# Kernel tuning notes

Hardware: AMD Instinct MI355X
Metric: run time of the kernel (lower is better)

## Reference

```python
import jax, jax.numpy as jnp
import numpy as np

HW = 1048576   # h*w pixels (1024x1024)
C = 64         # feature channels
K = 4096       # number of superpixel clusters (min_superpixels)
H1 = 256       # KAN hidden width
NCLS = 16      # output classes
G = 5          # grid_size
SO = 3         # spline_order


def _grid(in_features):
    # torch: (arange(-SO, G+SO+1) * h + grid_range[0]).expand(in_features, -1)
    h = 2.0 / G  # (grid_range[1]-grid_range[0])/grid_size
    g = jnp.arange(-SO, G + SO + 1, dtype=jnp.float32) * h - 1.0  # [G+2*SO+1]
    return jnp.broadcast_to(g, (in_features, G + 2 * SO + 1))


def _b_splines(x, grid):
    # x: [N, in] -> bases: [N, in, G+SO]
    xg = x[:, :, None]
    bases = ((xg >= grid[:, :-1]) & (xg < grid[:, 1:])).astype(x.dtype)
    for k in range(1, SO + 1):
        left = (xg - grid[:, :-(k + 1)]) / (grid[:, k:-1] - grid[:, :-(k + 1)])
        right = (grid[:, k + 1:] - xg) / (grid[:, k + 1:] - grid[:, 1:-k])
        bases = left * bases[:, :, :-1] + right * bases[:, :, 1:]
    return bases


def _kan_layer(x, base_w, spline_w, spline_scaler):
    # KANLinear.forward: silu(x) @ base_w.T + bsplines(x) . (spline_w * scaler)
    grid = _grid(x.shape[-1])
    base_out = jax.nn.silu(x) @ base_w.T                      # [N, out]
    bases = _b_splines(x, grid)                               # [N, in, G+SO]
    scaled_w = spline_w * spline_scaler[:, :, None]           # [out, in, G+SO]
    spline_out = jnp.einsum('nig,oig->no', bases, scaled_w)
    return base_out + spline_out


def setup_inputs() -> dict:
    key = jax.random.key(0)
    ks = jax.random.split(key, 8)
    x = jax.random.normal(ks[0], (HW, C), dtype=jnp.float32)
    cls = jax.random.randint(ks[1], (HW,), 0, K, dtype=jnp.int32)
    bw1 = jax.random.normal(ks[2], (H1, C), dtype=jnp.float32) * 0.1
    sw1 = jax.random.normal(ks[3], (H1, C, G + SO), dtype=jnp.float32) * 0.1
    sc1 = jax.random.normal(ks[4], (H1, C), dtype=jnp.float32) * 0.1
    bw2 = jax.random.normal(ks[5], (NCLS, H1), dtype=jnp.float32) * 0.1
    sw2 = jax.random.normal(ks[6], (NCLS, H1, G + SO), dtype=jnp.float32) * 0.1
    sc2 = jax.random.normal(ks[7], (NCLS, H1), dtype=jnp.float32) * 0.1
    return dict(x=x, cls=cls, bw1=bw1, sw1=sw1, sc1=sc1, bw2=bw2, sw2=sw2, sc2=sc2)


def reference(x, cls, bw1, sw1, sc1, bw2, sw2, sc2):
    # VDSM scatter-mean aggregation: per-cluster mean of pixel features
    sums = jax.ops.segment_sum(x, cls, num_segments=K)                       # [K, C]
    cnt = jax.ops.segment_sum(jnp.ones((HW,), x.dtype), cls, num_segments=K)  # [K]
    clus_feat = sums / jnp.maximum(cnt, 1.0)[:, None]
    # WIC_Cls: stack of KANLinear layers on cluster features
    h = _kan_layer(clus_feat, bw1, sw1, sc1)
    out = _kan_layer(h, bw2, sw2, sc2)
    return out
```

## Files before the change

kernel.cpp:

```cpp
#include <hip/hip_runtime.h>

#define HW_N 1048576
#define C_IN 64
#define K_CLS 4096
#define H1_N 256
#define NCLS_N 16
#define SCAT_BLOCKS 256
#define ROWS_PER_SCAT (HW_N / SCAT_BLOCKS)
#define CAP 512
#define CLPB 8

__device__ __forceinline__ float silu_f(float x) {
  return x / (1.0f + expf(-x));
}

__device__ __forceinline__ void bspline8(float x, float* b) {
  float t[11];
#pragma unroll
  for (int j = 0; j < 11; ++j) {
    float g0 = 0.4f * (float)(j - 3) - 1.0f;
    float g1 = 0.4f * (float)(j - 2) - 1.0f;
    t[j] = (x >= g0 && x < g1) ? 1.0f : 0.0f;
  }
#pragma unroll
  for (int k = 1; k <= 3; ++k) {
#pragma unroll 10
    for (int j = 0; j + k < 11; ++j) {
      float gj   = 0.4f * (float)(j - 3) - 1.0f;
      float gj1  = 0.4f * (float)(j - 2) - 1.0f;
      float gjk  = 0.4f * (float)(j + k - 3) - 1.0f;
      float gjk1 = 0.4f * (float)(j + k - 2) - 1.0f;
      float left  = (x - gj) / (gjk - gj);
      float right = (gjk1 - x) / (gjk1 - gj1);
      t[j] = left * t[j] + right * t[j + 1];
    }
  }
#pragma unroll
  for (int g = 0; g < 8; ++g) b[g] = t[g];
}

__global__ __launch_bounds__(256) void transpose_w(
    const float* __restrict__ bw1, const float* __restrict__ sw1,
    const float* __restrict__ sc1, const float* __restrict__ bw2,
    const float* __restrict__ sw2, const float* __restrict__ sc2,
    float* __restrict__ bwt1, float* __restrict__ swt1,
    float* __restrict__ bwt2, float* __restrict__ swt2,
    int* __restrict__ ccnt) {
  int bid = blockIdx.x, tid = threadIdx.x;
  if (bid < C_IN) {
    int i = bid, o = tid;
    float sc = sc1[o * C_IN + i];
    bwt1[i * H1_N + o] = bw1[o * C_IN + i];
    const float4* src = (const float4*)&sw1[(size_t)(o * C_IN + i) * 8];
    float4 a = src[0], b = src[1];
    a.x *= sc; a.y *= sc; a.z *= sc; a.w *= sc;
    b.x *= sc; b.y *= sc; b.z *= sc; b.w *= sc;
    float4* dst = (float4*)&swt1[(size_t)(i * H1_N + o) * 8];
    dst[0] = a; dst[1] = b;
  } else if (bid < C_IN + H1_N / 2) {
    int gi = (bid - C_IN) * 2 + (tid >> 7);
    int t = tid & 127;
    int o = t >> 3, e = t & 7;
    swt2[(gi * NCLS_N + o) * 8 + e] =
        sw2[(size_t)(o * H1_N + gi) * 8 + e] * sc2[o * H1_N + gi];
    if (t < NCLS_N) bwt2[gi * NCLS_N + t] = bw2[t * H1_N + gi];
  } else {
    ccnt[(bid - C_IN - H1_N / 2) * 256 + tid] = 0;
  }
}

__global__ __launch_bounds__(1024) void scatter_atomic(
    const int* __restrict__ cls, int* __restrict__ ccnt,
    int* __restrict__ spk) {
  __shared__ int lhist[K_CLS];
  int b = blockIdx.x, tid = threadIdx.x;
  for (int c = tid; c < K_CLS; c += 1024) lhist[c] = 0;
  __syncthreads();
  int r0 = b * ROWS_PER_SCAT;
  for (int r = r0 + tid; r < r0 + ROWS_PER_SCAT; r += 1024)
    atomicAdd(&lhist[cls[r]], 1);
  __syncthreads();
  for (int c = tid; c < K_CLS; c += 1024) {
    int n = lhist[c];
    lhist[c] = n ? atomicAdd(&ccnt[c], n) : 0;
  }
  __syncthreads();
  for (int r = r0 + tid; r < r0 + ROWS_PER_SCAT; r += 1024) {
    int c = cls[r];
    int pos = atomicAdd(&lhist[c], 1);
    spk[(size_t)c * CAP + pos] = r;
  }
}

__global__ __launch_bounds__(512, 4) void mega(
    const float* __restrict__ x, const int* __restrict__ spk,
    const int* __restrict__ ccnt, const float* __restrict__ bwt1,
    const float* __restrict__ swt1, const float* __restrict__ bwt2,
    const float* __restrict__ swt2, float* __restrict__ out) {
  __shared__ float s_bases[8][516];
  __shared__ float s_silu[8][65];
  __shared__ float mean_sacc[8][65];
  __shared__ float h_lds[8][257];
  __shared__ int sn[8];

  int bid = blockIdx.x, tid = threadIdx.x;
  int wv = tid >> 6, lane = tid & 63;
  int g = lane >> 4, q = lane & 15;

  if (tid < CLPB) sn[tid] = ccnt[bid * CLPB + tid];
  __syncthreads();

  {
    int n = sn[wv];
    const int* sid = spk + (size_t)(bid * CLPB + wv) * CAP;
    const float4* x4 = (const float4*)x;
    float ax = 0.0f, ay = 0.0f, az = 0.0f, aw = 0.0f;
    int i = g;
    for (; i + 28 < n; i += 32) {
      int p0 = sid[i],      p1 = sid[i + 4],  p2 = sid[i + 8],  p3 = sid[i + 12];
      int p4 = sid[i + 16], p5 = sid[i + 20], p6 = sid[i + 24], p7 = sid[i + 28];
      float4 v0 = x4[(size_t)p0 * 16 + q];
      float4 v1 = x4[(size_t)p1 * 16 + q];
      float4 v2 = x4[(size_t)p2 * 16 + q];
      float4 v3 = x4[(size_t)p3 * 16 + q];
      float4 v4 = x4[(size_t)p4 * 16 + q];
      float4 v5 = x4[(size_t)p5 * 16 + q];
      float4 v6 = x4[(size_t)p6 * 16 + q];
      float4 v7 = x4[(size_t)p7 * 16 + q];
      float tx0 = v0.x + v1.x, tx1 = v2.x + v3.x, tx2 = v4.x + v5.x, tx3 = v6.x + v7.x;
      float ty0 = v0.y + v1.y, ty1 = v2.y + v3.y, ty2 = v4.y + v5.y, ty3 = v6.y + v7.y;
      float tz0 = v0.z + v1.z, tz1 = v2.z + v3.z, tz2 = v4.z + v5.z, tz3 = v6.z + v7.z;
      float tw0 = v0.w + v1.w, tw1 = v2.w + v3.w, tw2 = v4.w + v5.w, tw3 = v6.w + v7.w;
      ax += (tx0 + tx1) + (tx2 + tx3);
      ay += (ty0 + ty1) + (ty2 + ty3);
      az += (tz0 + tz1) + (tz2 + tz3);
      aw += (tw0 + tw1) + (tw2 + tw3);
    }
    if (i < n) {
      int nm1 = n - 1;
      int i1 = i + 4, i2 = i + 8, i3 = i + 12, i4 = i + 16, i5 = i + 20,
          i6 = i + 24, i7 = i + 28;
      int p0 = sid[i];
      int p1 = sid[i1 < nm1 ? i1 : nm1];
      int p2 = sid[i2 < nm1 ? i2 : nm1];
      int p3 = sid[i3 < nm1 ? i3 : nm1];
      int p4 = sid[i4 < nm1 ? i4 : nm1];
      int p5 = sid[i5 < nm1 ? i5 : nm1];
      int p6 = sid[i6 < nm1 ? i6 : nm1];
      int p7 = sid[i7 < nm1 ? i7 : nm1];
      float4 v0 = x4[(size_t)p0 * 16 + q];
      float4 v1 = x4[(size_t)p1 * 16 + q];
      float4 v2 = x4[(size_t)p2 * 16 + q];
      float4 v3 = x4[(size_t)p3 * 16 + q];
      float4 v4 = x4[(size_t)p4 * 16 + q];
      float4 v5 = x4[(size_t)p5 * 16 + q];
      float4 v6 = x4[(size_t)p6 * 16 + q];
      float4 v7 = x4[(size_t)p7 * 16 + q];
      ax += v0.x; ay += v0.y; az += v0.z; aw += v0.w;
      if (i1 < n) { ax += v1.x; ay += v1.y; az += v1.z; aw += v1.w; }
      if (i2 < n) { ax += v2.x; ay += v2.y; az += v2.z; aw += v2.w; }
      if (i3 < n) { ax += v3.x; ay += v3.y; az += v3.z; aw += v3.w; }
      if (i4 < n) { ax += v4.x; ay += v4.y; az += v4.z; aw += v4.w; }
      if (i5 < n) { ax += v5.x; ay += v5.y; az += v5.z; aw += v5.w; }
      if (i6 < n) { ax += v6.x; ay += v6.y; az += v6.z; aw += v6.w; }
      if (i7 < n) { ax += v7.x; ay += v7.y; az += v7.z; aw += v7.w; }
    }
    ax += __shfl_xor(ax, 16); ax += __shfl_xor(ax, 32);
    ay += __shfl_xor(ay, 16); ay += __shfl_xor(ay, 32);
    az += __shfl_xor(az, 16); az += __shfl_xor(az, 32);
    aw += __shfl_xor(aw, 16); aw += __shfl_xor(aw, 32);
    if (g == 0) {
      float inv = 1.0f / fmaxf((float)n, 1.0f);
      mean_sacc[wv][q * 4 + 0] = ax * inv;
      mean_sacc[wv][q * 4 + 1] = ay * inv;
      mean_sacc[wv][q * 4 + 2] = az * inv;
      mean_sacc[wv][q * 4 + 3] = aw * inv;
    }
  }
  __syncthreads();

  {
    int r = tid >> 6, i = tid & 63;
    float xv = mean_sacc[r][i];
    s_silu[r][i] = silu_f(xv);
    float b[8];
    bspline8(xv, b);
    float4* dst = (float4*)&s_bases[r][i * 8];
    dst[0] = make_float4(b[0], b[1], b[2], b[3]);
    dst[1] = make_float4(b[4], b[5], b[6], b[7]);
  }
  __syncthreads();

  {
    int o = tid & 255, ih = tid >> 8;
    float acc[8];
#pragma unroll
    for (int r = 0; r < 8; ++r) acc[r] = 0.0f;
    int i0 = ih * 32;
    for (int i = i0; i < i0 + 32; ++i) {
      float wb = bwt1[i * H1_N + o];
      const float4* wp = (const float4*)&swt1[(size_t)(i * H1_N + o) * 8];
      float4 w0 = wp[0], w1 = wp[1];
#pragma unroll
      for (int r = 0; r < 8; ++r) {
        float sv = s_silu[r][i];
        const float4* bp = (const float4*)&s_bases[r][i * 8];
        float4 b0 = bp[0], b1 = bp[1];
        float a = acc[r];
        a = fmaf(sv, wb, a);
        a = fmaf(b0.x, w0.x, a); a = fmaf(b0.y, w0.y, a);
        a = fmaf(b0.z, w0.z, a); a = fmaf(b0.w, w0.w, a);
        a = fmaf(b1.x, w1.x, a); a = fmaf(b1.y, w1.y, a);
        a = fmaf(b1.z, w1.z, a); a = fmaf(b1.w, w1.w, a);
        acc[r] = a;
      }
    }
    if (ih == 0) {
#pragma unroll
      for (int r = 0; r < 8; ++r) h_lds[r][o] = acc[r];
    }
    __syncthreads();
    if (ih == 1) {
#pragma unroll
      for (int r = 0; r < 8; ++r) h_lds[r][o] += acc[r];
    }
  }
  __syncthreads();

  {
    int o2 = tid & 15, rr = (tid >> 4) & 7, jh = tid >> 7;
    float acc2 = 0.0f;
    for (int ic0 = 0; ic0 < H1_N; ic0 += 64) {
      {
        int r = tid >> 6, i = tid & 63;
        float xv = h_lds[r][ic0 + i];
        s_silu[r][i] = silu_f(xv);
        float b[8];
        bspline8(xv, b);
        float4* dst = (float4*)&s_bases[r][i * 8];
        dst[0] = make_float4(b[0], b[1], b[2], b[3]);
        dst[1] = make_float4(b[4], b[5], b[6], b[7]);
      }
      __syncthreads();
      int ib = jh * 16;
      for (int i = ib; i < ib + 16; ++i) {
        int gi = ic0 + i;
        float wb = bwt2[gi * NCLS_N + o2];
        const float4* wp = (const float4*)&swt2[(gi * NCLS_N + o2) * 8];
        float4 w0 = wp[0], w1 = wp[1];
        float sv = s_silu[rr][i];
        const float4* bp = (const float4*)&s_bases[rr][i * 8];
        float4 b0 = bp[0], b1 = bp[1];
        float sp = b0.x * w0.x + b0.y * w0.y + b0.z * w0.z + b0.w * w0.w
                 + b1.x * w1.x + b1.y * w1.y + b1.z * w1.z + b1.w * w1.w;
        acc2 = fmaf(sv, wb, acc2);
        acc2 += sp;
      }
      __syncthreads();
    }
    float* sac = &mean_sacc[0][0];
    sac[jh * 128 + rr * 16 + o2] = acc2;
    __syncthreads();
    if (tid < 128) {
      float s = sac[tid] + sac[128 + tid] + sac[256 + tid] + sac[384 + tid];
      out[(bid * CLPB + (tid >> 4)) * NCLS_N + (tid & 15)] = s;
    }
  }
}

extern "C" void kernel_launch(void* const* d_in, const int* in_sizes, int n_in,
                              void* d_out, int out_size, void* d_ws, size_t ws_size,
                              hipStream_t stream) {
  const float* x   = (const float*)d_in[0];
  const int*   cls = (const int*)d_in[1];
  const float* bw1 = (const float*)d_in[2];
  const float* sw1 = (const float*)d_in[3];
  const float* sc1 = (const float*)d_in[4];
  const float* bw2 = (const float*)d_in[5];
  const float* sw2 = (const float*)d_in[6];
  const float* sc2 = (const float*)d_in[7];
  float* out = (float*)d_out;

  int*   ccnt = (int*)d_ws;
  int*   spk  = ccnt + K_CLS;
  float* swt1 = (float*)(spk + K_CLS * CAP);
  float* bwt1 = swt1 + C_IN * H1_N * 8;
  float* swt2 = bwt1 + C_IN * H1_N;
  float* bwt2 = swt2 + H1_N * NCLS_N * 8;

  transpose_w<<<C_IN + H1_N / 2 + K_CLS / 256, 256, 0, stream>>>(
      bw1, sw1, sc1, bw2, sw2, sc2, bwt1, swt1, bwt2, swt2, ccnt);
  scatter_atomic<<<SCAT_BLOCKS, 1024, 0, stream>>>(cls, ccnt, spk);
  mega<<<K_CLS / CLPB, 512, 0, stream>>>(
      x, spk, ccnt, bwt1, swt1, bwt2, swt2, out);
}
```

Baseline: 128.3 us.

## Halve clusters per block, split each cluster gather across two waves

Each block now handles 4 clusters instead of 8, and two wavefronts cooperate on each cluster's pixel gather, combining partial sums through LDS float atomics. The KAN layer loops are resized to the smaller cluster count, the launch bound asks for 8 blocks per CU, and the scatter pass uses twice as many blocks. The goal is more blocks in flight and more memory-level parallelism for the irregular gather. In exchange, each block loads the layer weights for fewer clusters, so weight traffic rises, and LDS atomics are added.

```diff
diff --git a/kernel.cpp b/kernel.cpp
--- a/kernel.cpp
+++ b/kernel.cpp
@@ -5,10 +5,10 @@
 #define K_CLS 4096
 #define H1_N 256
 #define NCLS_N 16
-#define SCAT_BLOCKS 256
+#define SCAT_BLOCKS 512
 #define ROWS_PER_SCAT (HW_N / SCAT_BLOCKS)
 #define CAP 512
-#define CLPB 8
+#define CLPB 4
 
 __device__ __forceinline__ float silu_f(float x) {
   return x / (1.0f + expf(-x));
@@ -92,33 +92,34 @@
   }
 }
 
-__global__ __launch_bounds__(512, 4) void mega(
+__global__ __launch_bounds__(512, 8) void mega(
     const float* __restrict__ x, const int* __restrict__ spk,
     const int* __restrict__ ccnt, const float* __restrict__ bwt1,
     const float* __restrict__ swt1, const float* __restrict__ bwt2,
     const float* __restrict__ swt2, float* __restrict__ out) {
-  __shared__ float s_bases[8][516];
-  __shared__ float s_silu[8][65];
-  __shared__ float mean_sacc[8][65];
-  __shared__ float h_lds[8][257];
-  __shared__ int sn[8];
+  __shared__ float s_bases[4][516];
+  __shared__ float s_silu[4][65];
+  __shared__ float mean_acc[4][65];
+  __shared__ float h_lds[4][257];
 
   int bid = blockIdx.x, tid = threadIdx.x;
   int wv = tid >> 6, lane = tid & 63;
   int g = lane >> 4, q = lane & 15;
-
-  if (tid < CLPB) sn[tid] = ccnt[bid * CLPB + tid];
+  int cc = wv >> 1, sw = wv & 1;
+
+  if (tid < CLPB * 65) ((float*)mean_acc)[tid] = 0.0f;
   __syncthreads();
 
   {
-    int n = sn[wv];
-    const int* sid = spk + (size_t)(bid * CLPB + wv) * CAP;
+    int cidx = bid * CLPB + cc;
+    int n = ccnt[cidx];
+    const int* sid = spk + (size_t)cidx * CAP;
     const float4* x4 = (const float4*)x;
     float ax = 0.0f, ay = 0.0f, az = 0.0f, aw = 0.0f;
-    int i = g;
-    for (; i + 28 < n; i += 32) {
-      int p0 = sid[i],      p1 = sid[i + 4],  p2 = sid[i + 8],  p3 = sid[i + 12];
-      int p4 = sid[i + 16], p5 = sid[i + 20], p6 = sid[i + 24], p7 = sid[i + 28];
+    int i = sw * 4 + g;
+    for (; i + 56 < n; i += 64) {
+      int p0 = sid[i],      p1 = sid[i + 8],  p2 = sid[i + 16], p3 = sid[i + 24];
+      int p4 = sid[i + 32], p5 = sid[i + 40], p6 = sid[i + 48], p7 = sid[i + 56];
       float4 v0 = x4[(size_t)p0 * 16 + q];
       float4 v1 = x4[(size_t)p1 * 16 + q];
       float4 v2 = x4[(size_t)p2 * 16 + q];
@@ -138,8 +139,8 @@
     }
     if (i < n) {
       int nm1 = n - 1;
-      int i1 = i + 4, i2 = i + 8, i3 = i + 12, i4 = i + 16, i5 = i + 20,
-          i6 = i + 24, i7 = i + 28;
+      int i1 = i + 8, i2 = i + 16, i3 = i + 24, i4 = i + 32, i5 = i + 40,
+          i6 = i + 48, i7 = i + 56;
       int p0 = sid[i];
       int p1 = sid[i1 < nm1 ? i1 : nm1];
       int p2 = sid[i2 < nm1 ? i2 : nm1];
@@ -170,18 +171,18 @@
     az += __shfl_xor(az, 16); az += __shfl_xor(az, 32);
     aw += __shfl_xor(aw, 16); aw += __shfl_xor(aw, 32);
     if (g == 0) {
-      float inv = 1.0f / fmaxf((float)n, 1.0f);
-      mean_sacc[wv][q * 4 + 0] = ax * inv;
-      mean_sacc[wv][q * 4 + 1] = ay * inv;
-      mean_sacc[wv][q * 4 + 2] = az * inv;
-      mean_sacc[wv][q * 4 + 3] = aw * inv;
-    }
-  }
-  __syncthreads();
-
-  {
+      atomicAdd(&mean_acc[cc][q * 4 + 0], ax);
+      atomicAdd(&mean_acc[cc][q * 4 + 1], ay);
+      atomicAdd(&mean_acc[cc][q * 4 + 2], az);
+      atomicAdd(&mean_acc[cc][q * 4 + 3], aw);
+    }
+  }
+  __syncthreads();
+
+  if (tid < CLPB * 64) {
     int r = tid >> 6, i = tid & 63;
-    float xv = mean_sacc[r][i];
+    float inv = 1.0f / fmaxf((float)ccnt[bid * CLPB + r], 1.0f);
+    float xv = mean_acc[r][i] * inv;
     s_silu[r][i] = silu_f(xv);
     float b[8];
     bspline8(xv, b);
@@ -193,16 +194,16 @@
 
   {
     int o = tid & 255, ih = tid >> 8;
-    float acc[8];
-#pragma unroll
-    for (int r = 0; r < 8; ++r) acc[r] = 0.0f;
+    float acc[4];
+#pragma unroll
+    for (int r = 0; r < 4; ++r) acc[r] = 0.0f;
     int i0 = ih * 32;
     for (int i = i0; i < i0 + 32; ++i) {
       float wb = bwt1[i * H1_N + o];
       const float4* wp = (const float4*)&swt1[(size_t)(i * H1_N + o) * 8];
       float4 w0 = wp[0], w1 = wp[1];
 #pragma unroll
-      for (int r = 0; r < 8; ++r) {
+      for (int r = 0; r < 4; ++r) {
         float sv = s_silu[r][i];
         const float4* bp = (const float4*)&s_bases[r][i * 8];
         float4 b0 = bp[0], b1 = bp[1];
@@ -217,21 +218,21 @@
     }
     if (ih == 0) {
 #pragma unroll
-      for (int r = 0; r < 8; ++r) h_lds[r][o] = acc[r];
+      for (int r = 0; r < 4; ++r) h_lds[r][o] = acc[r];
     }
     __syncthreads();
     if (ih == 1) {
 #pragma unroll
-      for (int r = 0; r < 8; ++r) h_lds[r][o] += acc[r];
+      for (int r = 0; r < 4; ++r) h_lds[r][o] += acc[r];
     }
   }
   __syncthreads();
 
   {
-    int o2 = tid & 15, rr = (tid >> 4) & 7, jh = tid >> 7;
+    int o2 = tid & 15, rr = (tid >> 4) & 3, jh = tid >> 6;
     float acc2 = 0.0f;
     for (int ic0 = 0; ic0 < H1_N; ic0 += 64) {
-      {
+      if (tid < CLPB * 64) {
         int r = tid >> 6, i = tid & 63;
         float xv = h_lds[r][ic0 + i];
         s_silu[r][i] = silu_f(xv);
@@ -242,8 +243,8 @@
         dst[1] = make_float4(b[4], b[5], b[6], b[7]);
       }
       __syncthreads();
-      int ib = jh * 16;
-      for (int i = ib; i < ib + 16; ++i) {
+      int ib = jh * 8;
+      for (int i = ib; i < ib + 8; ++i) {
         int gi = ic0 + i;
         float wb = bwt2[gi * NCLS_N + o2];
         const float4* wp = (const float4*)&swt2[(gi * NCLS_N + o2) * 8];
@@ -258,11 +259,13 @@
       }
       __syncthreads();
     }
-    float* sac = &mean_sacc[0][0];
-    sac[jh * 128 + rr * 16 + o2] = acc2;
+    float* sac = &s_bases[0][0];
+    sac[jh * 64 + rr * 16 + o2] = acc2;
     __syncthreads();
-    if (tid < 128) {
-      float s = sac[tid] + sac[128 + tid] + sac[256 + tid] + sac[384 + tid];
+    if (tid < 64) {
+      float s = 0.0f;
+#pragma unroll
+      for (int j = 0; j < 8; ++j) s += sac[j * 64 + tid];
       out[(bid * CLPB + (tid >> 4)) * NCLS_N + (tid & 15)] = s;
     }
   }
```

New measurement: 154.1 us. +20.1%, slower.
